# Kernel optimization log

Measured on AMD Instinct MI355X. Metric: run time of the kernel, lower is better.

The kernel has to match this reference:

```python
import jax, jax.numpy as jnp
import numpy as np

B, T, I, H, O = 64, 1024, 256, 512, 128


def setup_inputs() -> dict:
    key = jax.random.key(0)
    ks = jax.random.split(key, 12)
    s = 1.0 / np.sqrt(H)  # PyTorch LSTM init: U(-1/sqrt(H), 1/sqrt(H))
    u = lambda k, shape: jax.random.uniform(k, shape, jnp.float32, -s, s)
    return {
        "inputs": jax.random.normal(ks[0], (B, T, I), jnp.float32),
        "W_ih_f": u(ks[1], (4 * H, I)),
        "W_hh_f": u(ks[2], (4 * H, H)),
        "b_ih_f": u(ks[3], (4 * H,)),
        "b_hh_f": u(ks[4], (4 * H,)),
        "W_ih_b": u(ks[5], (4 * H, I)),
        "W_hh_b": u(ks[6], (4 * H, H)),
        "b_ih_b": u(ks[7], (4 * H,)),
        "b_hh_b": u(ks[8], (4 * H,)),
        "W_out": u(ks[9], (O, 2 * H)),
        "b_out": u(ks[10], (O,)),
    }


def _lstm_dir(inputs, W_ih, W_hh, b_ih, b_hh, reverse):
    # Precompute input contribution for all timesteps: [B,T,4H] -> [T,B,4H]
    xg = jnp.einsum("bti,gi->btg", inputs, W_ih) + b_ih + b_hh
    xg = jnp.swapaxes(xg, 0, 1)
    b = inputs.shape[0]
    h0 = jnp.zeros((b, H), inputs.dtype)
    c0 = jnp.zeros((b, H), inputs.dtype)

    def step(carry, x_t):
        h, c = carry
        gates = x_t + h @ W_hh.T  # [B,4H], PyTorch gate order i,f,g,o
        i, f, g, o = jnp.split(gates, 4, axis=-1)
        i = jax.nn.sigmoid(i)
        f = jax.nn.sigmoid(f)
        g = jnp.tanh(g)
        o = jax.nn.sigmoid(o)
        c = f * c + i * g
        h = o * jnp.tanh(c)
        return (h, c), h

    (hT, cT), hs = jax.lax.scan(step, (h0, c0), xg, reverse=reverse)
    return jnp.swapaxes(hs, 0, 1), hT, cT  # hs: [B,T,H]


def reference(inputs, W_ih_f, W_hh_f, b_ih_f, b_hh_f,
              W_ih_b, W_hh_b, b_ih_b, b_hh_b, W_out, b_out):
    y_f, h_f, c_f = _lstm_dir(inputs, W_ih_f, W_hh_f, b_ih_f, b_hh_f, False)
    y_b, h_b, c_b = _lstm_dir(inputs, W_ih_b, W_hh_b, b_ih_b, b_hh_b, True)
    y = jnp.concatenate([y_f, y_b], axis=-1)            # [B,T,2H]
    out = jnp.einsum("bth,oh->bto", y, W_out) + b_out    # [B,T,O]
    h_n = jnp.stack([h_f, h_b])                          # [2,B,H]
    c_n = jnp.stack([c_f, c_b])                          # [2,B,H]
    return out, h_n, c_n
```

## Files before the change

kernel.cpp:

```cpp
#include <hip/hip_runtime.h>
#include <stdint.h>

#define T_LEN 1024
#define B_SZ  64
#define I_SZ  256
#define H_SZ  512
#define O_SZ  128

#define FLAG_OFF 0ull
#define HB_OFF  524288ull
#define Y_OFF   786432ull
#define XBF_OFF 135004160ull
#define MEMSET_BYTES 786432ull

typedef __attribute__((ext_vector_type(8))) short short8;
typedef __attribute__((ext_vector_type(4))) float f32x4;

__device__ __forceinline__ unsigned short f2bf(float f) {
  unsigned u = __float_as_uint(f);
  u += 0x7fffu + ((u >> 16) & 1u);
  return (unsigned short)(u >> 16);
}
__device__ __forceinline__ ushort4 cvt4(float4 v) {
  ushort4 p;
  p.x = f2bf(v.x); p.y = f2bf(v.y); p.z = f2bf(v.z); p.w = f2bf(v.w);
  return p;
}
__device__ __forceinline__ float sigm(float x) { return 1.0f / (1.0f + __expf(-x)); }
__device__ __forceinline__ float tanh_f(float x) { return 1.0f - 2.0f / (1.0f + __expf(2.0f * x)); }

__global__ void __launch_bounds__(256) cvt_x(const float* __restrict__ x,
                                             unsigned short* __restrict__ xb) {
  size_t i = ((size_t)blockIdx.x * 256 + threadIdx.x) * 8;
  float4 a = *(const float4*)(x + i);
  float4 b = *(const float4*)(x + i + 4);
  *(ushort4*)(xb + i)     = cvt4(a);
  *(ushort4*)(xb + i + 4) = cvt4(b);
}

__global__ void __launch_bounds__(512, 2)
lstm_scan(const unsigned short* __restrict__ xbf,
          const float* __restrict__ WihF, const float* __restrict__ WhhF,
          const float* __restrict__ bihF, const float* __restrict__ bhhF,
          const float* __restrict__ WihB, const float* __restrict__ WhhB,
          const float* __restrict__ bihB, const float* __restrict__ bhhB,
          unsigned char* __restrict__ ws, float* __restrict__ out)
{
  __shared__ unsigned short xs[2][32][264];
  __shared__ unsigned short hs[32][520];
  __shared__ float gbuf[4][32][18];
  __shared__ float cst[32][18];

  const int tid  = threadIdx.x;
  const int lane = tid & 63;
  const int wave = tid >> 6;
  const int nl   = lane & 15;
  const int q16  = lane >> 4;

  const int wg   = blockIdx.x;
  const int d    = wg >> 6;
  const int loc  = wg & 63;
  const int b0   = (loc >> 5) * 32;
  const int u0   = (loc & 31) * 16;
  const int grp  = wg >> 5;
  const int wgid = loc & 31;

  const float* Wih = d ? WihB : WihF;
  const float* Whh = d ? WhhB : WhhF;
  const float* bih = d ? bihB : bihF;
  const float* bhh = d ? bhhB : bhhF;

  const int gate = wave >> 1;
  const int mt   = wave & 1;

  short8 wfrag[24];
  {
    const int row = gate * H_SZ + u0 + nl;
    const float* wi = Wih + (size_t)row * I_SZ;
    const float* wh = Whh + (size_t)row * H_SZ;
#pragma unroll
    for (int kk = 0; kk < 24; ++kk) {
      const float* src = (kk < 8) ? (wi + kk * 32 + q16 * 8)
                                  : (wh + (kk - 8) * 32 + q16 * 8);
      float4 v0 = ((const float4*)src)[0];
      float4 v1 = ((const float4*)src)[1];
      short8 w;
      w[0] = (short)f2bf(v0.x); w[1] = (short)f2bf(v0.y);
      w[2] = (short)f2bf(v0.z); w[3] = (short)f2bf(v0.w);
      w[4] = (short)f2bf(v1.x); w[5] = (short)f2bf(v1.y);
      w[6] = (short)f2bf(v1.z); w[7] = (short)f2bf(v1.w);
      wfrag[kk] = w;
    }
  }
  const float bias = bih[gate * H_SZ + u0 + nl] + bhh[gate * H_SZ + u0 + nl];

  cst[tid >> 4][tid & 15] = 0.0f;

  unsigned* flags  = (unsigned*)(ws + FLAG_OFF);
  unsigned* hbuf32 = (unsigned*)(ws + HB_OFF);
  unsigned* ybuf32 = (unsigned*)(ws + Y_OFF);
  unsigned* hs32   = (unsigned*)hs;

  const int sm = tid >> 4, sseg = tid & 15;

  {
    const int t0 = d ? (T_LEN - 1) : 0;
    const uint4* src = (const uint4*)(xbf + ((size_t)(b0 + sm) * T_LEN + t0) * I_SZ + sseg * 16);
    uint4 a = src[0], b = src[1];
    uint4* dst = (uint4*)(&xs[0][sm][sseg * 16]);
    dst[0] = a; dst[1] = b;
  }
  __syncthreads();
  f32x4 xacc = {0.f, 0.f, 0.f, 0.f};
  {
    const unsigned short* xr = &xs[0][mt * 16 + nl][q16 * 8];
#pragma unroll
    for (int kk = 0; kk < 8; ++kk) {
      short8 a = *(const short8*)(xr + kk * 32);
      xacc = __builtin_amdgcn_mfma_f32_16x16x32_bf16(a, wfrag[kk], xacc, 0, 0, 0);
    }
  }
  uint4 px0, px1;
  {
    const int t1 = d ? (T_LEN - 2) : 1;
    const uint4* src = (const uint4*)(xbf + ((size_t)(b0 + sm) * T_LEN + t1) * I_SZ + sseg * 16);
    px0 = src[0]; px1 = src[1];
  }

  for (int s = 0; s < T_LEN; ++s) {
    const int t   = d ? (T_LEN - 1 - s) : s;
    const int cur = s & 1, nxt = cur ^ 1;
    const int rb  = cur ^ 1, wb = cur;

    if (s > 0) {
      const unsigned tgt = (unsigned)s;
      unsigned* fl = flags + grp * 32;
      for (;;) {
        unsigned f = (lane < 32)
          ? __hip_atomic_load(fl + lane, __ATOMIC_RELAXED, __HIP_MEMORY_SCOPE_AGENT)
          : tgt;
        if (__all((int)(f >= tgt))) break;
      }
    }

    {
      unsigned hv[16];
      unsigned* hb = hbuf32 + (size_t)((rb * 2 + d) * B_SZ + b0) * 256;
#pragma unroll
      for (int j = 0; j < 16; ++j)
        hv[j] = __hip_atomic_load(hb + j * 512 + tid, __ATOMIC_RELAXED, __HIP_MEMORY_SCOPE_AGENT);
#pragma unroll
      for (int j = 0; j < 16; ++j) {
        int lin = j * 512 + tid;
        hs32[(lin >> 8) * 260 + (lin & 255)] = hv[j];
      }
    }
    __syncthreads();

    f32x4 acc0 = xacc, acc1 = {0.f, 0.f, 0.f, 0.f};
    {
      const unsigned short* ar = &hs[mt * 16 + nl][q16 * 8];
#pragma unroll
      for (int kk = 0; kk < 16; kk += 2) {
        short8 a0 = *(const short8*)(ar + kk * 32);
        short8 a1 = *(const short8*)(ar + (kk + 1) * 32);
        acc0 = __builtin_amdgcn_mfma_f32_16x16x32_bf16(a0, wfrag[8 + kk], acc0, 0, 0, 0);
        acc1 = __builtin_amdgcn_mfma_f32_16x16x32_bf16(a1, wfrag[9 + kk], acc1, 0, 0, 0);
      }
      acc0 += acc1;
    }

#pragma unroll
    for (int r = 0; r < 4; ++r) {
      float v = acc0[r] + bias;
      v = (gate == 2) ? tanh_f(v) : sigm(v);
      gbuf[gate][mt * 16 + q16 * 4 + r][nl] = v;
    }
    __syncthreads();

    {
      int m = tid >> 4, n = tid & 15;
      float gi = gbuf[0][m][n], gf = gbuf[1][m][n];
      float gg = gbuf[2][m][n], go = gbuf[3][m][n];
      float c = gf * cst[m][n] + gi * gg;
      cst[m][n] = c;
      float h = go * tanh_f(c);
      unsigned hbits = f2bf(h);
      unsigned other = __shfl_xor(hbits, 1);
      if ((tid & 1) == 0) {
        unsigned packed = hbits | (other << 16);
        size_t hi = (size_t)((wb * 2 + d) * B_SZ + b0 + m) * 256 + (u0 + n) / 2;
        __hip_atomic_store(hbuf32 + hi, packed, __ATOMIC_RELAXED, __HIP_MEMORY_SCOPE_AGENT);
        size_t yi = ((size_t)(b0 + m) * T_LEN + t) * 512 + (d * H_SZ + u0 + n) / 2;
        ybuf32[yi] = packed;
      }
      if (s == T_LEN - 1) {
        size_t hi = (size_t)(d * B_SZ + b0 + m) * H_SZ + u0 + n;
        out[8388608ull + hi] = h;
        out[8388608ull + 65536ull + hi] = c;
      }
    }

    if (s < T_LEN - 1) {
      uint4* dst = (uint4*)(&xs[nxt][sm][sseg * 16]);
      dst[0] = px0; dst[1] = px1;
    }
    __builtin_amdgcn_s_waitcnt(0);
    __syncthreads();

    if (s < T_LEN - 1) {
      if (tid == 0)
        __hip_atomic_store(flags + grp * 32 + wgid, (unsigned)(s + 1),
                           __ATOMIC_RELAXED, __HIP_MEMORY_SCOPE_AGENT);
      if (s + 2 < T_LEN) {
        const int t2 = d ? (T_LEN - 3 - s) : (s + 2);
        const uint4* src = (const uint4*)(xbf + ((size_t)(b0 + sm) * T_LEN + t2) * I_SZ + sseg * 16);
        px0 = src[0]; px1 = src[1];
      }
      f32x4 xa = {0.f, 0.f, 0.f, 0.f};
      const unsigned short* xr = &xs[nxt][mt * 16 + nl][q16 * 8];
#pragma unroll
      for (int kk = 0; kk < 8; ++kk) {
        short8 a = *(const short8*)(xr + kk * 32);
        xa = __builtin_amdgcn_mfma_f32_16x16x32_bf16(a, wfrag[kk], xa, 0, 0, 0);
      }
      xacc = xa;
    }
  }
}

__global__ void __launch_bounds__(256, 1)
proj(const unsigned short* __restrict__ y, const float* __restrict__ Wout,
     const float* __restrict__ bout, float* __restrict__ out)
{
  __shared__ unsigned short ys[128 * 264];
  __shared__ unsigned short wst[128 * 264];

  const int tid  = threadIdx.x;
  const int wave = tid >> 6;
  const int lane = tid & 63;
  const int nl   = lane & 15;
  const int q16  = lane >> 4;
  const int m0   = blockIdx.x * 128;

  f32x4 acc[2][8];
#pragma unroll
  for (int a = 0; a < 2; ++a)
#pragma unroll
    for (int b = 0; b < 8; ++b) acc[a][b] = (f32x4){0.f, 0.f, 0.f, 0.f};

  for (int k0 = 0; k0 < 1024; k0 += 256) {
    {
      int r = tid >> 1, half = tid & 1;
      const uint4* src = (const uint4*)(y + (size_t)(m0 + r) * 1024 + k0 + half * 128);
      uint4* dst = (uint4*)(ys + r * 264 + half * 128);
#pragma unroll
      for (int q = 0; q < 16; ++q) dst[q] = src[q];
    }
    {
      int r = tid >> 1, half = tid & 1;
      const float4* src = (const float4*)(Wout + (size_t)r * 1024 + k0 + half * 128);
      unsigned short* wd = wst + r * 264 + half * 128;
#pragma unroll
      for (int q = 0; q < 32; ++q) *(ushort4*)(wd + q * 4) = cvt4(src[q]);
    }
    __syncthreads();

#pragma unroll
    for (int kk = 0; kk < 8; ++kk) {
      const int ko = kk * 32 + q16 * 8;
      short8 bfr[8];
#pragma unroll
      for (int nt = 0; nt < 8; ++nt)
        bfr[nt] = *(const short8*)(wst + (nt * 16 + nl) * 264 + ko);
#pragma unroll
      for (int mtt = 0; mtt < 2; ++mtt) {
        short8 a = *(const short8*)(ys + ((wave * 2 + mtt) * 16 + nl) * 264 + ko);
#pragma unroll
        for (int nt = 0; nt < 8; ++nt)
          acc[mtt][nt] = __builtin_amdgcn_mfma_f32_16x16x32_bf16(a, bfr[nt], acc[mtt][nt], 0, 0, 0);
      }
    }
    __syncthreads();
  }

#pragma unroll
  for (int mtt = 0; mtt < 2; ++mtt) {
#pragma unroll
    for (int nt = 0; nt < 8; ++nt) {
      int col = nt * 16 + nl;
      float bo = bout[col];
      int rowb = m0 + (wave * 2 + mtt) * 16 + q16 * 4;
#pragma unroll
      for (int r = 0; r < 4; ++r)
        out[(size_t)(rowb + r) * O_SZ + col] = acc[mtt][nt][r] + bo;
    }
  }
}

extern "C" void kernel_launch(void* const* d_in, const int* in_sizes, int n_in,
                              void* d_out, int out_size, void* d_ws, size_t ws_size,
                              hipStream_t stream) {
  const float* x    = (const float*)d_in[0];
  const float* WihF = (const float*)d_in[1];
  const float* WhhF = (const float*)d_in[2];
  const float* bihF = (const float*)d_in[3];
  const float* bhhF = (const float*)d_in[4];
  const float* WihB = (const float*)d_in[5];
  const float* WhhB = (const float*)d_in[6];
  const float* bihB = (const float*)d_in[7];
  const float* bhhB = (const float*)d_in[8];
  const float* Wout = (const float*)d_in[9];
  const float* bout = (const float*)d_in[10];
  float* out = (float*)d_out;
  unsigned char* ws = (unsigned char*)d_ws;

  hipMemsetAsync(ws, 0, (size_t)MEMSET_BYTES, stream);
  cvt_x<<<8192, 256, 0, stream>>>(x, (unsigned short*)(ws + XBF_OFF));
  lstm_scan<<<128, 512, 0, stream>>>((const unsigned short*)(ws + XBF_OFF),
                                     WihF, WhhF, bihF, bhhF,
                                     WihB, WhhB, bihB, bhhB,
                                     ws, out);
  proj<<<512, 256, 0, stream>>>((const unsigned short*)(ws + Y_OFF), Wout, bout, out);
}
```

Before: 3.375 ms.

## Retile LSTM scan to 16 batch rows by 32 units per workgroup

Changes the per-workgroup tile from 32 batch rows by 16 hidden units to 16 batch rows by 32 units. Each direction/batch group now syncs over 16 workgroups instead of 32, and each workgroup reads half as much h state per step. The y-output store moves after the flag publish so the waitcnt before signaling no longer waits on it. The x staging store is also hoisted into the h-load phase. This cuts per-step global h traffic and flag-polling fan-in, at the cost of more groups (8) and smaller per-WG batch tiles.

```diff
diff --git a/kernel.cpp b/kernel.cpp
--- a/kernel.cpp
+++ b/kernel.cpp
@@ -8,10 +8,10 @@
 #define O_SZ  128
 
 #define FLAG_OFF 0ull
-#define HB_OFF  524288ull
-#define Y_OFF   786432ull
-#define XBF_OFF 135004160ull
-#define MEMSET_BYTES 786432ull
+#define HB_OFF  65536ull
+#define Y_OFF   327680ull
+#define XBF_OFF 134545408ull
+#define MEMSET_BYTES 327680ull
 
 typedef __attribute__((ext_vector_type(8))) short short8;
 typedef __attribute__((ext_vector_type(4))) float f32x4;
@@ -46,10 +46,10 @@
           const float* __restrict__ bihB, const float* __restrict__ bhhB,
           unsigned char* __restrict__ ws, float* __restrict__ out)
 {
-  __shared__ unsigned short xs[2][32][264];
-  __shared__ unsigned short hs[32][520];
-  __shared__ float gbuf[4][32][18];
-  __shared__ float cst[32][18];
+  __shared__ unsigned short xs[2][16][264];
+  __shared__ unsigned short hs[16][520];
+  __shared__ float gbuf[4][16][36];
+  __shared__ float cst[16][36];
 
   const int tid  = threadIdx.x;
   const int lane = tid & 63;
@@ -59,11 +59,10 @@
 
   const int wg   = blockIdx.x;
   const int d    = wg >> 6;
-  const int loc  = wg & 63;
-  const int b0   = (loc >> 5) * 32;
-  const int u0   = (loc & 31) * 16;
-  const int grp  = wg >> 5;
-  const int wgid = loc & 31;
+  const int b0   = ((wg >> 4) & 3) * 16;
+  const int u0   = (wg & 15) * 32;
+  const int grp  = wg >> 4;
+  const int wgid = wg & 15;
 
   const float* Wih = d ? WihB : WihF;
   const float* Whh = d ? WhhB : WhhF;
@@ -71,11 +70,11 @@
   const float* bhh = d ? bhhB : bhhF;
 
   const int gate = wave >> 1;
-  const int mt   = wave & 1;
+  const int usub = (wave & 1) * 16;
 
   short8 wfrag[24];
   {
-    const int row = gate * H_SZ + u0 + nl;
+    const int row = gate * H_SZ + u0 + usub + nl;
     const float* wi = Wih + (size_t)row * I_SZ;
     const float* wh = Whh + (size_t)row * H_SZ;
 #pragma unroll
@@ -92,39 +91,36 @@
       wfrag[kk] = w;
     }
   }
-  const float bias = bih[gate * H_SZ + u0 + nl] + bhh[gate * H_SZ + u0 + nl];
-
-  cst[tid >> 4][tid & 15] = 0.0f;
+  const float bias = bih[gate * H_SZ + u0 + usub + nl] + bhh[gate * H_SZ + u0 + usub + nl];
+
+  cst[tid >> 5][tid & 31] = 0.0f;
 
   unsigned* flags  = (unsigned*)(ws + FLAG_OFF);
   unsigned* hbuf32 = (unsigned*)(ws + HB_OFF);
   unsigned* ybuf32 = (unsigned*)(ws + Y_OFF);
   unsigned* hs32   = (unsigned*)hs;
 
-  const int sm = tid >> 4, sseg = tid & 15;
+  const int sm = tid >> 5, sseg = tid & 31;
 
   {
     const int t0 = d ? (T_LEN - 1) : 0;
-    const uint4* src = (const uint4*)(xbf + ((size_t)(b0 + sm) * T_LEN + t0) * I_SZ + sseg * 16);
-    uint4 a = src[0], b = src[1];
-    uint4* dst = (uint4*)(&xs[0][sm][sseg * 16]);
-    dst[0] = a; dst[1] = b;
+    uint4 a = *(const uint4*)(xbf + ((size_t)(b0 + sm) * T_LEN + t0) * I_SZ + sseg * 8);
+    *(uint4*)(&xs[0][sm][sseg * 8]) = a;
   }
   __syncthreads();
   f32x4 xacc = {0.f, 0.f, 0.f, 0.f};
   {
-    const unsigned short* xr = &xs[0][mt * 16 + nl][q16 * 8];
+    const unsigned short* xr = &xs[0][nl][q16 * 8];
 #pragma unroll
     for (int kk = 0; kk < 8; ++kk) {
       short8 a = *(const short8*)(xr + kk * 32);
       xacc = __builtin_amdgcn_mfma_f32_16x16x32_bf16(a, wfrag[kk], xacc, 0, 0, 0);
     }
   }
-  uint4 px0, px1;
+  uint4 px;
   {
     const int t1 = d ? (T_LEN - 2) : 1;
-    const uint4* src = (const uint4*)(xbf + ((size_t)(b0 + sm) * T_LEN + t1) * I_SZ + sseg * 16);
-    px0 = src[0]; px1 = src[1];
+    px = *(const uint4*)(xbf + ((size_t)(b0 + sm) * T_LEN + t1) * I_SZ + sseg * 8);
   }
 
   for (int s = 0; s < T_LEN; ++s) {
@@ -134,9 +130,9 @@
 
     if (s > 0) {
       const unsigned tgt = (unsigned)s;
-      unsigned* fl = flags + grp * 32;
+      const unsigned* fl = flags + grp * 16;
       for (;;) {
-        unsigned f = (lane < 32)
+        unsigned f = (lane < 16)
           ? __hip_atomic_load(fl + lane, __ATOMIC_RELAXED, __HIP_MEMORY_SCOPE_AGENT)
           : tgt;
         if (__all((int)(f >= tgt))) break;
@@ -144,13 +140,15 @@
     }
 
     {
-      unsigned hv[16];
-      unsigned* hb = hbuf32 + (size_t)((rb * 2 + d) * B_SZ + b0) * 256;
-#pragma unroll
-      for (int j = 0; j < 16; ++j)
+      unsigned hv[8];
+      const unsigned* hb = hbuf32 + (size_t)((rb * 2 + d) * B_SZ + b0) * 256;
+#pragma unroll
+      for (int j = 0; j < 8; ++j)
         hv[j] = __hip_atomic_load(hb + j * 512 + tid, __ATOMIC_RELAXED, __HIP_MEMORY_SCOPE_AGENT);
-#pragma unroll
-      for (int j = 0; j < 16; ++j) {
+      if (s < T_LEN - 1)
+        *(uint4*)(&xs[nxt][sm][sseg * 8]) = px;
+#pragma unroll
+      for (int j = 0; j < 8; ++j) {
         int lin = j * 512 + tid;
         hs32[(lin >> 8) * 260 + (lin & 255)] = hv[j];
       }
@@ -159,7 +157,7 @@
 
     f32x4 acc0 = xacc, acc1 = {0.f, 0.f, 0.f, 0.f};
     {
-      const unsigned short* ar = &hs[mt * 16 + nl][q16 * 8];
+      const unsigned short* ar = &hs[nl][q16 * 8];
 #pragma unroll
       for (int kk = 0; kk < 16; kk += 2) {
         short8 a0 = *(const short8*)(ar + kk * 32);
@@ -174,12 +172,13 @@
     for (int r = 0; r < 4; ++r) {
       float v = acc0[r] + bias;
       v = (gate == 2) ? tanh_f(v) : sigm(v);
-      gbuf[gate][mt * 16 + q16 * 4 + r][nl] = v;
+      gbuf[gate][q16 * 4 + r][usub + nl] = v;
     }
     __syncthreads();
 
-    {
-      int m = tid >> 4, n = tid & 15;
+    unsigned packed; size_t yi;
+    {
+      int m = tid >> 5, n = tid & 31;
       float gi = gbuf[0][m][n], gf = gbuf[1][m][n];
       float gg = gbuf[2][m][n], go = gbuf[3][m][n];
       float c = gf * cst[m][n] + gi * gg;
@@ -187,12 +186,11 @@
       float h = go * tanh_f(c);
       unsigned hbits = f2bf(h);
       unsigned other = __shfl_xor(hbits, 1);
+      packed = hbits | (other << 16);
+      yi = ((size_t)(b0 + m) * T_LEN + t) * 512 + (d * H_SZ + u0 + n) / 2;
       if ((tid & 1) == 0) {
-        unsigned packed = hbits | (other << 16);
         size_t hi = (size_t)((wb * 2 + d) * B_SZ + b0 + m) * 256 + (u0 + n) / 2;
         __hip_atomic_store(hbuf32 + hi, packed, __ATOMIC_RELAXED, __HIP_MEMORY_SCOPE_AGENT);
-        size_t yi = ((size_t)(b0 + m) * T_LEN + t) * 512 + (d * H_SZ + u0 + n) / 2;
-        ybuf32[yi] = packed;
       }
       if (s == T_LEN - 1) {
         size_t hi = (size_t)(d * B_SZ + b0 + m) * H_SZ + u0 + n;
@@ -202,23 +200,23 @@
     }
 
     if (s < T_LEN - 1) {
-      uint4* dst = (uint4*)(&xs[nxt][sm][sseg * 16]);
-      dst[0] = px0; dst[1] = px1;
-    }
-    __builtin_amdgcn_s_waitcnt(0);
-    __syncthreads();
+      __builtin_amdgcn_s_waitcnt(0);
+      __syncthreads();
+      if (tid == 0)
+        __hip_atomic_store(flags + grp * 16 + wgid, (unsigned)(s + 1),
+                           __ATOMIC_RELAXED, __HIP_MEMORY_SCOPE_AGENT);
+    }
+
+    if ((tid & 1) == 0)
+      ybuf32[yi] = packed;
 
     if (s < T_LEN - 1) {
-      if (tid == 0)
-        __hip_atomic_store(flags + grp * 32 + wgid, (unsigned)(s + 1),
-                           __ATOMIC_RELAXED, __HIP_MEMORY_SCOPE_AGENT);
       if (s + 2 < T_LEN) {
         const int t2 = d ? (T_LEN - 3 - s) : (s + 2);
-        const uint4* src = (const uint4*)(xbf + ((size_t)(b0 + sm) * T_LEN + t2) * I_SZ + sseg * 16);
-        px0 = src[0]; px1 = src[1];
+        px = *(const uint4*)(xbf + ((size_t)(b0 + sm) * T_LEN + t2) * I_SZ + sseg * 8);
       }
       f32x4 xa = {0.f, 0.f, 0.f, 0.f};
-      const unsigned short* xr = &xs[nxt][mt * 16 + nl][q16 * 8];
+      const unsigned short* xr = &xs[nxt][nl][q16 * 8];
 #pragma unroll
       for (int kk = 0; kk < 8; ++kk) {
         short8 a = *(const short8*)(xr + kk * 32);
```

Result: slower. 3.798 ms (+12.5%).
